# Optimization experiments

Hardware: AMD Instinct MI355X
Metric: run time of the kernel (lower is better)

Reference implementation:

```python
import jax, jax.numpy as jnp
import numpy as np
import math

B, S, H = 8, 160, 768
DEP = 64
NH, DH = 12, H // 12
W_EDGE = 1.0
EPS = 1e-5


def setup_inputs() -> dict:
    key = jax.random.key(0)
    ks = jax.random.split(key, 16)
    sc_h = 1.0 / math.sqrt(H)
    sc_d = 1.0 / math.sqrt(DEP)
    return {
        "token_feature": jax.random.normal(ks[0], (B, S, H), jnp.float32),
        "edge_feature": jax.random.normal(ks[1], (B, S, S, DEP), jnp.float32),
        "dependency_masks": jax.random.randint(ks[2], (B, S, S), 0, 2, jnp.int32),
        "Wq": jax.random.normal(ks[3], (H, H), jnp.float32) * sc_h,
        "bq": jnp.zeros((H,), jnp.float32),
        "Wk": jax.random.normal(ks[4], (H, H), jnp.float32) * sc_h,
        "bk": jnp.zeros((H,), jnp.float32),
        "Wv": jax.random.normal(ks[5], (H, H), jnp.float32) * sc_h,
        "bv": jnp.zeros((H,), jnp.float32),
        "Wek": jax.random.normal(ks[6], (DEP, H), jnp.float32) * sc_d,
        "bek": jnp.zeros((H,), jnp.float32),
        "Wev": jax.random.normal(ks[7], (DEP, H), jnp.float32) * sc_d,
        "bev": jnp.zeros((H,), jnp.float32),
        "ln_g": jnp.ones((H,), jnp.float32),
        "ln_b": jnp.zeros((H,), jnp.float32),
    }


def _heads3(x):  # [B,S,H] -> [B,NH,S,DH]
    return x.reshape(B, S, NH, DH).transpose(0, 2, 1, 3)


def _heads4(x):  # [B,S,S,H] -> [B,NH,S,S,DH]
    return x.reshape(B, S, S, NH, DH).transpose(0, 3, 1, 2, 4)


def reference(token_feature, edge_feature, dependency_masks,
              Wq, bq, Wk, bk, Wv, bv, Wek, bek, Wev, bev, ln_g, ln_b):
    q = _heads3(token_feature @ Wq + bq)   # [B,NH,S,DH]
    k = _heads3(token_feature @ Wk + bk)
    v = _heads3(token_feature @ Wv + bv)
    ek = _heads4(edge_feature @ Wek + bek)  # [B,NH,S,S,DH]
    ev = _heads4(edge_feature @ Wev + bev)
    # key_ij = k_j + w*ek_ij ; scores_ij = q_i . key_ij / sqrt(dh)
    scores = (jnp.einsum('bhid,bhjd->bhij', q, k)
              + W_EDGE * jnp.einsum('bhid,bhijd->bhij', q, ek))
    scores = scores / math.sqrt(DH)
    mask = (dependency_masks[:, None, :, :] == 0)  # [B,1,S,S]
    scores = jnp.where(mask, jnp.float32(-10000.0), scores)
    probs = jax.nn.softmax(scores, axis=-1)  # dropout is identity in eval
    ctx = (jnp.einsum('bhij,bhjd->bhid', probs, v)
           + W_EDGE * jnp.einsum('bhij,bhijd->bhid', probs, ev))
    ctx = ctx.transpose(0, 2, 1, 3).reshape(B, S, H)
    x = token_feature + ctx
    mu = jnp.mean(x, axis=-1, keepdims=True)
    var = jnp.mean(jnp.square(x - mu), axis=-1, keepdims=True)
    return (x - mu) / jnp.sqrt(var + EPS) * ln_g + ln_b
```

## Files before the change

kernel.cpp:

```cpp
#include <hip/hip_runtime.h>
#include <hip/hip_bf16.h>
#include <math.h>

#define BB 8
#define SS 160
#define HH 768
#define DEPTH 64
#define NHEAD 12
#define DHEAD 64
#define BS (BB*SS)
#define SCROW (NHEAD*SS)

constexpr float EPS_C = 1e-5f;

typedef __attribute__((ext_vector_type(8))) short bf16x8;
typedef __attribute__((ext_vector_type(4))) float f32x4;

__device__ inline short f2bs(float x) {
    union { __hip_bfloat16 b; short s; } u;
    u.b = __float2bfloat16(x);
    return u.s;
}

__global__ __launch_bounds__(256) void transpose_cast_w(
    const float* __restrict__ Wq, const float* __restrict__ Wk,
    const float* __restrict__ Wv, __hip_bfloat16* __restrict__ WT)
{
    __shared__ float t[32][33];
    const float* W = (blockIdx.z == 0) ? Wq : (blockIdx.z == 1) ? Wk : Wv;
    __hip_bfloat16* o = WT + (size_t)blockIdx.z * HH * HH;
    int kt = blockIdx.x * 32, nt = blockIdx.y * 32;
    int tx = threadIdx.x & 31, ty = threadIdx.x >> 5;
#pragma unroll
    for (int r = 0; r < 32; r += 8)
        t[ty + r][tx] = W[(size_t)(kt + ty + r) * HH + nt + tx];
    __syncthreads();
#pragma unroll
    for (int r = 0; r < 32; r += 8)
        o[(size_t)(nt + ty + r) * HH + kt + tx] = __float2bfloat16(t[tx][ty + r]);
}

__global__ __launch_bounds__(256) void gemm_qkv(
    const float* __restrict__ X, const __hip_bfloat16* __restrict__ WT,
    const float* __restrict__ bq, const float* __restrict__ bk,
    const float* __restrict__ bv,
    __hip_bfloat16* __restrict__ qb, __hip_bfloat16* __restrict__ kb,
    __hip_bfloat16* __restrict__ vb)
{
    __shared__ int4 sA[4][128];
    __shared__ int4 sB[4][64];
    int m0 = blockIdx.x * 128, n0 = blockIdx.y * 64, mat = blockIdx.z;
    const short* W = (const short*)WT + (size_t)mat * HH * HH;
    const float* bias = (mat == 0) ? bq : (mat == 1) ? bk : bv;
    int tid = threadIdx.x, w = tid >> 6, l = tid & 63;
    int wm = (w >> 1) * 64, wn = (w & 1) * 32;
    int khalf = l >> 4, lc = l & 15;

    f32x4 acc[4][2];
#pragma unroll
    for (int i = 0; i < 4; i++)
#pragma unroll
        for (int j = 0; j < 2; j++) acc[i][j] = (f32x4){0.f, 0.f, 0.f, 0.f};

    for (int k0 = 0; k0 < HH; k0 += 32) {
        __syncthreads();
#pragma unroll
        for (int rr = 0; rr < 2; rr++) {
            const float* ap = X + (size_t)(m0 + l + rr * 64) * HH + k0 + w * 8;
            float4 x0 = *(const float4*)ap;
            float4 x1 = *(const float4*)(ap + 4);
            bf16x8 p;
            p[0]=f2bs(x0.x); p[1]=f2bs(x0.y); p[2]=f2bs(x0.z); p[3]=f2bs(x0.w);
            p[4]=f2bs(x1.x); p[5]=f2bs(x1.y); p[6]=f2bs(x1.z); p[7]=f2bs(x1.w);
            *(bf16x8*)&sA[w][l + rr * 64] = p;
        }
        sB[w][l] = *(const int4*)(W + (size_t)(n0 + l) * HH + k0 + w * 8);
        __syncthreads();
        bf16x8 b0 = *(const bf16x8*)&sB[khalf][wn + lc];
        bf16x8 b1 = *(const bf16x8*)&sB[khalf][wn + 16 + lc];
#pragma unroll
        for (int mi = 0; mi < 4; mi++) {
            bf16x8 a = *(const bf16x8*)&sA[khalf][wm + mi * 16 + lc];
            acc[mi][0] = __builtin_amdgcn_mfma_f32_16x16x32_bf16(a, b0, acc[mi][0], 0, 0, 0);
            acc[mi][1] = __builtin_amdgcn_mfma_f32_16x16x32_bf16(a, b1, acc[mi][1], 0, 0, 0);
        }
    }

    int rg = (l >> 4) * 4;
    __hip_bfloat16* outm = (mat == 0) ? qb : (mat == 1) ? kb : vb;
#pragma unroll
    for (int ni = 0; ni < 2; ni++) {
        int gcol = n0 + wn + ni * 16 + lc;
        float bv_ = bias[gcol];
#pragma unroll
        for (int mi = 0; mi < 4; mi++) {
            int grow = m0 + wm + mi * 16 + rg;
            f32x4 a = acc[mi][ni];
            __hip_bfloat16* o = outm + (size_t)grow * HH + gcol;
            o[0]      = __float2bfloat16(a.x + bv_);
            o[HH]     = __float2bfloat16(a.y + bv_);
            o[2 * HH] = __float2bfloat16(a.z + bv_);
            o[3 * HH] = __float2bfloat16(a.w + bv_);
        }
    }
}

__global__ __launch_bounds__(256) void scores_gemm(
    const __hip_bfloat16* __restrict__ qb, const __hip_bfloat16* __restrict__ kb,
    _Float16* __restrict__ sc)
{
    __shared__ int4 sQ[8][160];
    __shared__ int4 sK[8][160];
    int h = blockIdx.x, b = blockIdx.y;
    const short* Q = (const short*)qb + (size_t)b * SS * HH + h * DHEAD;
    const short* K = (const short*)kb + (size_t)b * SS * HH + h * DHEAD;
    int tid = threadIdx.x, w = tid >> 6, l = tid & 63;

    for (int idx = tid; idx < SS * 8; idx += 256) {
        int row = idx >> 3, ch = idx & 7;
        sQ[ch][row] = *(const int4*)(Q + (size_t)row * HH + ch * 8);
        sK[ch][row] = *(const int4*)(K + (size_t)row * HH + ch * 8);
    }
    __syncthreads();

    int wm = (w >> 1) * 80, wn = (w & 1) * 80;
    int khalf = l >> 4, lc = l & 15;
    f32x4 acc[5][5];
#pragma unroll
    for (int i = 0; i < 5; i++)
#pragma unroll
        for (int j = 0; j < 5; j++) acc[i][j] = (f32x4){0.f, 0.f, 0.f, 0.f};

#pragma unroll
    for (int s = 0; s < 2; s++) {
        int c = s * 4 + khalf;
        bf16x8 bf[5];
#pragma unroll
        for (int ni = 0; ni < 5; ni++)
            bf[ni] = *(const bf16x8*)&sK[c][wn + ni * 16 + lc];
#pragma unroll
        for (int mi = 0; mi < 5; mi++) {
            bf16x8 a = *(const bf16x8*)&sQ[c][wm + mi * 16 + lc];
#pragma unroll
            for (int ni = 0; ni < 5; ni++)
                acc[mi][ni] = __builtin_amdgcn_mfma_f32_16x16x32_bf16(a, bf[ni], acc[mi][ni], 0, 0, 0);
        }
    }

    int rg = (l >> 4) * 4;
    _Float16* base = sc + ((size_t)b * SS) * SCROW + (size_t)h * SS;
#pragma unroll
    for (int mi = 0; mi < 5; mi++) {
        int i0 = wm + mi * 16 + rg;
#pragma unroll
        for (int ni = 0; ni < 5; ni++) {
            int j = wn + ni * 16 + lc;
            f32x4 a = acc[mi][ni];
            base[(size_t)(i0 + 0) * SCROW + j] = (_Float16)(a.x * 0.125f);
            base[(size_t)(i0 + 1) * SCROW + j] = (_Float16)(a.y * 0.125f);
            base[(size_t)(i0 + 2) * SCROW + j] = (_Float16)(a.z * 0.125f);
            base[(size_t)(i0 + 3) * SCROW + j] = (_Float16)(a.w * 0.125f);
        }
    }
}

__global__ __launch_bounds__(256) void qek_slim(
    const __hip_bfloat16* __restrict__ qb, const float* __restrict__ Wek,
    __hip_bfloat16* __restrict__ qek)
{
    __shared__ short sW[8 * 65 * 8];
    int h = blockIdx.x, mg = blockIdx.y;
    int tid = threadIdx.x, w = tid >> 6, l = tid & 63;
    int lr = l & 15, kg = l >> 4;

    {
        int d = tid >> 2, q4 = tid & 3;
        const float* wp = Wek + (size_t)d * HH + h * DHEAD + q4 * 16;
        float4 w0 = *(const float4*)(wp);
        float4 w1 = *(const float4*)(wp + 4);
        float4 w2 = *(const float4*)(wp + 8);
        float4 w3 = *(const float4*)(wp + 12);
        bf16x8 p0, p1;
        p0[0]=f2bs(w0.x); p0[1]=f2bs(w0.y); p0[2]=f2bs(w0.z); p0[3]=f2bs(w0.w);
        p0[4]=f2bs(w1.x); p0[5]=f2bs(w1.y); p0[6]=f2bs(w1.z); p0[7]=f2bs(w1.w);
        p1[0]=f2bs(w2.x); p1[1]=f2bs(w2.y); p1[2]=f2bs(w2.z); p1[3]=f2bs(w2.w);
        p1[4]=f2bs(w3.x); p1[5]=f2bs(w3.y); p1[6]=f2bs(w3.z); p1[7]=f2bs(w3.w);
        *(bf16x8*)&sW[((q4 * 2) * 65 + d) * 8]     = p0;
        *(bf16x8*)&sW[((q4 * 2 + 1) * 65 + d) * 8] = p1;
    }
    __syncthreads();

    bf16x8 bfrag[2][4];
#pragma unroll
    for (int s = 0; s < 2; s++)
#pragma unroll
        for (int nt = 0; nt < 4; nt++)
            bfrag[s][nt] = *(const bf16x8*)&sW[((s * 4 + kg) * 65 + nt * 16 + lr) * 8];

    const short* Q = (const short*)qb;
    short* O = (short*)qek;
    int m0 = (mg * 4 + w) * 16;
    bf16x8 a0 = *(const bf16x8*)(Q + (size_t)(m0 + lr) * HH + h * DHEAD + kg * 8);
    bf16x8 a1 = *(const bf16x8*)(Q + (size_t)(m0 + lr) * HH + h * DHEAD + 32 + kg * 8);
#pragma unroll
    for (int nt = 0; nt < 4; nt++) {
        f32x4 acc = (f32x4){0.f, 0.f, 0.f, 0.f};
        acc = __builtin_amdgcn_mfma_f32_16x16x32_bf16(a0, bfrag[0][nt], acc, 0, 0, 0);
        acc = __builtin_amdgcn_mfma_f32_16x16x32_bf16(a1, bfrag[1][nt], acc, 0, 0, 0);
        int row0 = m0 + kg * 4;
#pragma unroll
        for (int r = 0; r < 4; r++)
            O[(size_t)(row0 + r) * HH + h * DHEAD + nt * 16 + lr] = f2bs(acc[r]);
    }
}

__global__ __launch_bounds__(256) void escore_add2(
    const float* __restrict__ edge, const __hip_bfloat16* __restrict__ qek,
    _Float16* __restrict__ sc)
{
    int task = blockIdx.x * 4 + (threadIdx.x >> 6);
    int l = threadIdx.x & 63;
    int bi = task / 5, seg = task - (task / 5) * 5;
    int lr = l & 15, kg = l >> 4;

    const short* QE = (const short*)qek + (size_t)bi * HH;
    bf16x8 qe0 = *(const bf16x8*)(QE + lr * DHEAD + kg * 8);
    bf16x8 qe1 = *(const bf16x8*)(QE + lr * DHEAD + 32 + kg * 8);

    const float* E = edge + (size_t)bi * SS * DEPTH;
    _Float16* srow = sc + (size_t)bi * SCROW;

#pragma unroll
    for (int t = 0; t < 2; t++) {
        int jt = seg * 2 + t;
        const float* ep = E + (size_t)(jt * 16 + lr) * DEPTH + kg * 8;
        float4 e0 = *(const float4*)(ep);
        float4 e1 = *(const float4*)(ep + 4);
        float4 e2 = *(const float4*)(ep + 32);
        float4 e3 = *(const float4*)(ep + 36);
        bf16x8 a0, a1;
        a0[0]=f2bs(e0.x); a0[1]=f2bs(e0.y); a0[2]=f2bs(e0.z); a0[3]=f2bs(e0.w);
        a0[4]=f2bs(e1.x); a0[5]=f2bs(e1.y); a0[6]=f2bs(e1.z); a0[7]=f2bs(e1.w);
        a1[0]=f2bs(e2.x); a1[1]=f2bs(e2.y); a1[2]=f2bs(e2.z); a1[3]=f2bs(e2.w);
        a1[4]=f2bs(e3.x); a1[5]=f2bs(e3.y); a1[6]=f2bs(e3.z); a1[7]=f2bs(e3.w);
        f32x4 acc = (f32x4){0.f, 0.f, 0.f, 0.f};
        acc = __builtin_amdgcn_mfma_f32_16x16x32_bf16(a0, qe0, acc, 0, 0, 0);
        acc = __builtin_amdgcn_mfma_f32_16x16x32_bf16(a1, qe1, acc, 0, 0, 0);
        if (lr < NHEAD) {
            int j0 = jt * 16 + kg * 4;
            _Float16* p = srow + (size_t)lr * SS + j0;
#pragma unroll
            for (int r = 0; r < 4; r++)
                p[r] = (_Float16)((float)p[r] + 0.125f * acc[r]);
        }
    }
}

__global__ __launch_bounds__(256) void attn_kernel(
    const float* __restrict__ token, const float* __restrict__ edge,
    const int* __restrict__ mask,
    const __hip_bfloat16* __restrict__ q_ws, const _Float16* __restrict__ sc,
    const __hip_bfloat16* __restrict__ v_ws,
    const float* __restrict__ bek,
    const float* __restrict__ Wev, const float* __restrict__ bev,
    const float* __restrict__ ln_g, const float* __restrict__ ln_b,
    float* __restrict__ out)
{
    __shared__ float  s_ctx[HH];
    __shared__ float  s_scores[NHEAD][SS + 2];
    __shared__ float  s_pe[NHEAD][DEPTH];
    __shared__ float  s_x[HH];
    __shared__ float  s_qbek[NHEAD];
    __shared__ int    s_mask[SS];
    __shared__ float  s_red[8];

    int bi = blockIdx.x;
    int b  = bi / SS;
    int tid = threadIdx.x;
    int w = tid >> 6, l = tid & 63;
    int lr = l & 15, kg = l >> 4;

    if (tid < SS) s_mask[tid] = mask[(size_t)bi * SS + tid];

    {
        int hs = w * 3 + kg;
        float part = 0.f;
        if (hs < NHEAD) {
            const __hip_bfloat16* qp = q_ws + (size_t)bi * HH + hs * DHEAD + lr * 4;
            float4 bv4 = *(const float4*)(bek + hs * DHEAD + lr * 4);
            part = __bfloat162float(qp[0]) * bv4.x + __bfloat162float(qp[1]) * bv4.y
                 + __bfloat162float(qp[2]) * bv4.z + __bfloat162float(qp[3]) * bv4.w;
        }
        part += __shfl_xor(part, 1, 64);
        part += __shfl_xor(part, 2, 64);
        part += __shfl_xor(part, 4, 64);
        part += __shfl_xor(part, 8, 64);
        if (lr == 0 && hs < NHEAD) s_qbek[hs] = part;
    }
    __syncthreads();

    const float* scf = (const float*)(sc + (size_t)bi * SCROW);
    for (int idx = tid; idx < SCROW / 2; idx += 256) {
        int h = idx / (SS / 2), jp = idx - h * (SS / 2);
        union { float f; _Float16 e[2]; } u;
        u.f = scf[idx];
        int j = jp * 2;
        s_scores[h][j]     = s_mask[j]     ? ((float)u.e[0] + 0.125f * s_qbek[h]) : -10000.0f;
        s_scores[h][j + 1] = s_mask[j + 1] ? ((float)u.e[1] + 0.125f * s_qbek[h]) : -10000.0f;
    }
    __syncthreads();

    for (int h = w; h < NHEAD; h += 4) {
        float v0 = s_scores[h][l];
        float v1 = s_scores[h][l + 64];
        float v2 = (l < 32) ? s_scores[h][l + 128] : -INFINITY;
        float mx = fmaxf(v0, fmaxf(v1, v2));
#pragma unroll
        for (int mm = 32; mm >= 1; mm >>= 1) mx = fmaxf(mx, __shfl_xor(mx, mm, 64));
        float e0 = expf(v0 - mx), e1 = expf(v1 - mx);
        float e2 = (l < 32) ? expf(v2 - mx) : 0.f;
        float sm = e0 + e1 + e2;
#pragma unroll
        for (int mm = 32; mm >= 1; mm >>= 1) sm += __shfl_xor(sm, mm, 64);
        float inv = 1.0f / sm;
        s_scores[h][l]      = e0 * inv;
        s_scores[h][l + 64] = e1 * inv;
        if (l < 32) s_scores[h][l + 128] = e2 * inv;
    }
    __syncthreads();

    const float* e_row = edge + (size_t)bi * SS * DEPTH;
    {
        int h0 = w * 3;
        float av0 = 0.f, av1 = 0.f, av2 = 0.f;
        float pe0 = 0.f, pe1 = 0.f, pe2 = 0.f;
        const __hip_bfloat16* vbp = v_ws + (size_t)b * SS * HH + h0 * DHEAD + l;
        const float* er = e_row + l;
#pragma unroll 2
        for (int j0 = 0; j0 < SS; j0 += 2) {
            float2 p0 = *(const float2*)(&s_scores[h0][j0]);
            float2 p1 = *(const float2*)(&s_scores[h0 + 1][j0]);
            float2 p2 = *(const float2*)(&s_scores[h0 + 2][j0]);
            const __hip_bfloat16* vp = vbp + (size_t)j0 * HH;
            av0 += p0.x * __bfloat162float(vp[0])
                 + p0.y * __bfloat162float(vp[HH]);
            av1 += p1.x * __bfloat162float(vp[DHEAD])
                 + p1.y * __bfloat162float(vp[HH + DHEAD]);
            av2 += p2.x * __bfloat162float(vp[2 * DHEAD])
                 + p2.y * __bfloat162float(vp[HH + 2 * DHEAD]);
            float ev0 = er[(size_t)j0 * DEPTH];
            float ev1 = er[(size_t)(j0 + 1) * DEPTH];
            pe0 += p0.x * ev0 + p0.y * ev1;
            pe1 += p1.x * ev0 + p1.y * ev1;
            pe2 += p2.x * ev0 + p2.y * ev1;
        }
        s_pe[h0][l]     = pe0;
        s_pe[h0 + 1][l] = pe1;
        s_pe[h0 + 2][l] = pe2;
        s_ctx[h0 * DHEAD + l]       = av0;
        s_ctx[(h0 + 1) * DHEAD + l] = av1;
        s_ctx[(h0 + 2) * DHEAD + l] = av2;
    }
    __syncthreads();

    for (int mdx = tid; mdx < HH; mdx += 256) {
        int h = mdx >> 6;
        const float* pep = &s_pe[h][0];
        float sum = 0.f;
#pragma unroll
        for (int d = 0; d < DEPTH; d++) sum += pep[d] * Wev[(size_t)d * HH + mdx];
        float ctx = s_ctx[mdx] + (sum + bev[mdx]);
        s_x[mdx] = token[(size_t)bi * HH + mdx] + ctx;
    }
    __syncthreads();

    float lsum = 0.f, lsq = 0.f;
    for (int c = tid; c < HH; c += 256) {
        float x = s_x[c];
        lsum += x; lsq += x * x;
    }
#pragma unroll
    for (int mm = 32; mm >= 1; mm >>= 1) {
        lsum += __shfl_xor(lsum, mm, 64);
        lsq  += __shfl_xor(lsq,  mm, 64);
    }
    if (l == 0) { s_red[w] = lsum; s_red[4 + w] = lsq; }
    __syncthreads();
    float tsum = s_red[0] + s_red[1] + s_red[2] + s_red[3];
    float tsq  = s_red[4] + s_red[5] + s_red[6] + s_red[7];
    float mu  = tsum / HH;
    float var = tsq / HH - mu * mu;
    float rstd = rsqrtf(var + EPS_C);
    for (int c = tid; c < HH; c += 256)
        out[(size_t)bi * HH + c] = (s_x[c] - mu) * rstd * ln_g[c] + ln_b[c];
}

extern "C" void kernel_launch(void* const* d_in, const int* in_sizes, int n_in,
                              void* d_out, int out_size, void* d_ws, size_t ws_size,
                              hipStream_t stream) {
    const float* token = (const float*)d_in[0];
    const float* edge  = (const float*)d_in[1];
    const int*   mask  = (const int*)d_in[2];
    const float* Wq = (const float*)d_in[3];  const float* bq = (const float*)d_in[4];
    const float* Wk = (const float*)d_in[5];  const float* bk = (const float*)d_in[6];
    const float* Wv = (const float*)d_in[7];  const float* bv = (const float*)d_in[8];
    const float* Wek = (const float*)d_in[9];  const float* bek = (const float*)d_in[10];
    const float* Wev = (const float*)d_in[11]; const float* bev = (const float*)d_in[12];
    const float* ln_g = (const float*)d_in[13]; const float* ln_b = (const float*)d_in[14];
    float* out = (float*)d_out;

    __hip_bfloat16* qb = (__hip_bfloat16*)d_ws;
    __hip_bfloat16* kb = qb + (size_t)BS * HH;
    __hip_bfloat16* vb = kb + (size_t)BS * HH;
    __hip_bfloat16* WT = vb + (size_t)BS * HH;
    _Float16*       sc = (_Float16*)WT;
    __hip_bfloat16* qek = kb;

    transpose_cast_w<<<dim3(24, 24, 3), 256, 0, stream>>>(Wq, Wk, Wv, WT);
    gemm_qkv<<<dim3(BS / 128, HH / 64, 3), 256, 0, stream>>>(
        token, WT, bq, bk, bv, qb, kb, vb);
    scores_gemm<<<dim3(NHEAD, BB), 256, 0, stream>>>(qb, kb, sc);
    qek_slim<<<dim3(NHEAD, 20), 256, 0, stream>>>(qb, Wek, qek);
    escore_add2<<<1600, 256, 0, stream>>>(edge, qek, sc);
    attn_kernel<<<BS, 256, 0, stream>>>(token, edge, mask, qb, sc, vb,
                                        bek, Wev, bev, ln_g, ln_b, out);
}
```

Before: 119.1 us.

## Fuse weight transpose-cast into QKV GEMM and simplify attention loops

Drops the separate transpose_cast_w launch. The QKV GEMM now reads fp32 weights directly with strided per-column loads and converts them to bf16 while filling shared memory. The attention kernel now loads fp16 scores one element at a time instead of as packed pairs, and its PV/edge loop is rewritten to step one key per iteration with unroll 4 instead of two-key float2 steps. This saves a launch and the round trip of the transposed weight buffer, at the cost of strided, redundant fp32 weight reads in every GEMM tile and narrower memory accesses.

```diff
diff --git a/kernel.cpp b/kernel.cpp
--- a/kernel.cpp
+++ b/kernel.cpp
@@ -22,26 +22,10 @@
     return u.s;
 }
 
-__global__ __launch_bounds__(256) void transpose_cast_w(
+__global__ __launch_bounds__(256) void gemm_qkv(
+    const float* __restrict__ X,
     const float* __restrict__ Wq, const float* __restrict__ Wk,
-    const float* __restrict__ Wv, __hip_bfloat16* __restrict__ WT)
-{
-    __shared__ float t[32][33];
-    const float* W = (blockIdx.z == 0) ? Wq : (blockIdx.z == 1) ? Wk : Wv;
-    __hip_bfloat16* o = WT + (size_t)blockIdx.z * HH * HH;
-    int kt = blockIdx.x * 32, nt = blockIdx.y * 32;
-    int tx = threadIdx.x & 31, ty = threadIdx.x >> 5;
-#pragma unroll
-    for (int r = 0; r < 32; r += 8)
-        t[ty + r][tx] = W[(size_t)(kt + ty + r) * HH + nt + tx];
-    __syncthreads();
-#pragma unroll
-    for (int r = 0; r < 32; r += 8)
-        o[(size_t)(nt + ty + r) * HH + kt + tx] = __float2bfloat16(t[tx][ty + r]);
-}
-
-__global__ __launch_bounds__(256) void gemm_qkv(
-    const float* __restrict__ X, const __hip_bfloat16* __restrict__ WT,
+    const float* __restrict__ Wv,
     const float* __restrict__ bq, const float* __restrict__ bk,
     const float* __restrict__ bv,
     __hip_bfloat16* __restrict__ qb, __hip_bfloat16* __restrict__ kb,
@@ -50,7 +34,7 @@
     __shared__ int4 sA[4][128];
     __shared__ int4 sB[4][64];
     int m0 = blockIdx.x * 128, n0 = blockIdx.y * 64, mat = blockIdx.z;
-    const short* W = (const short*)WT + (size_t)mat * HH * HH;
+    const float* W    = (mat == 0) ? Wq : (mat == 1) ? Wk : Wv;
     const float* bias = (mat == 0) ? bq : (mat == 1) ? bk : bv;
     int tid = threadIdx.x, w = tid >> 6, l = tid & 63;
     int wm = (w >> 1) * 64, wn = (w & 1) * 32;
@@ -74,7 +58,13 @@
             p[4]=f2bs(x1.x); p[5]=f2bs(x1.y); p[6]=f2bs(x1.z); p[7]=f2bs(x1.w);
             *(bf16x8*)&sA[w][l + rr * 64] = p;
         }
-        sB[w][l] = *(const int4*)(W + (size_t)(n0 + l) * HH + k0 + w * 8);
+        {
+            const float* wp = W + (size_t)(k0 + w * 8) * HH + n0 + l;
+            bf16x8 p;
+#pragma unroll
+            for (int i = 0; i < 8; i++) p[i] = f2bs(wp[(size_t)i * HH]);
+            *(bf16x8*)&sB[w][l] = p;
+        }
         __syncthreads();
         bf16x8 b0 = *(const bf16x8*)&sB[khalf][wn + lc];
         bf16x8 b1 = *(const bf16x8*)&sB[khalf][wn + 16 + lc];
@@ -267,7 +257,7 @@
     float* __restrict__ out)
 {
     __shared__ float  s_ctx[HH];
-    __shared__ float  s_scores[NHEAD][SS + 2];
+    __shared__ float  s_scores[NHEAD][SS];
     __shared__ float  s_pe[NHEAD][DEPTH];
     __shared__ float  s_x[HH];
     __shared__ float  s_qbek[NHEAD];
@@ -299,14 +289,11 @@
     }
     __syncthreads();
 
-    const float* scf = (const float*)(sc + (size_t)bi * SCROW);
-    for (int idx = tid; idx < SCROW / 2; idx += 256) {
-        int h = idx / (SS / 2), jp = idx - h * (SS / 2);
-        union { float f; _Float16 e[2]; } u;
-        u.f = scf[idx];
-        int j = jp * 2;
-        s_scores[h][j]     = s_mask[j]     ? ((float)u.e[0] + 0.125f * s_qbek[h]) : -10000.0f;
-        s_scores[h][j + 1] = s_mask[j + 1] ? ((float)u.e[1] + 0.125f * s_qbek[h]) : -10000.0f;
+    const _Float16* scrow = sc + (size_t)bi * SCROW;
+    for (int idx = tid; idx < NHEAD * SS; idx += 256) {
+        int h = idx / SS, j = idx - h * SS;
+        float qk = (float)scrow[idx];
+        s_scores[h][j] = s_mask[j] ? (qk + 0.125f * s_qbek[h]) : -10000.0f;
     }
     __syncthreads();
 
@@ -336,23 +323,18 @@
         float pe0 = 0.f, pe1 = 0.f, pe2 = 0.f;
         const __hip_bfloat16* vbp = v_ws + (size_t)b * SS * HH + h0 * DHEAD + l;
         const float* er = e_row + l;
-#pragma unroll 2
-        for (int j0 = 0; j0 < SS; j0 += 2) {
-            float2 p0 = *(const float2*)(&s_scores[h0][j0]);
-            float2 p1 = *(const float2*)(&s_scores[h0 + 1][j0]);
-            float2 p2 = *(const float2*)(&s_scores[h0 + 2][j0]);
-            const __hip_bfloat16* vp = vbp + (size_t)j0 * HH;
-            av0 += p0.x * __bfloat162float(vp[0])
-                 + p0.y * __bfloat162float(vp[HH]);
-            av1 += p1.x * __bfloat162float(vp[DHEAD])
-                 + p1.y * __bfloat162float(vp[HH + DHEAD]);
-            av2 += p2.x * __bfloat162float(vp[2 * DHEAD])
-                 + p2.y * __bfloat162float(vp[HH + 2 * DHEAD]);
-            float ev0 = er[(size_t)j0 * DEPTH];
-            float ev1 = er[(size_t)(j0 + 1) * DEPTH];
-            pe0 += p0.x * ev0 + p0.y * ev1;
-            pe1 += p1.x * ev0 + p1.y * ev1;
-            pe2 += p2.x * ev0 + p2.y * ev1;
+        const float* p0r = &s_scores[h0][0];
+        const float* p1r = &s_scores[h0 + 1][0];
+        const float* p2r = &s_scores[h0 + 2][0];
+#pragma unroll 4
+        for (int j = 0; j < SS; j++) {
+            float p0 = p0r[j], p1 = p1r[j], p2 = p2r[j];
+            const __hip_bfloat16* vp = vbp + (size_t)j * HH;
+            av0 += p0 * __bfloat162float(vp[0]);
+            av1 += p1 * __bfloat162float(vp[DHEAD]);
+            av2 += p2 * __bfloat162float(vp[2 * DHEAD]);
+            float ev = er[(size_t)j * DEPTH];
+            pe0 += p0 * ev; pe1 += p1 * ev; pe2 += p2 * ev;
         }
         s_pe[h0][l]     = pe0;
         s_pe[h0 + 1][l] = pe1;
@@ -412,13 +394,11 @@
     __hip_bfloat16* qb = (__hip_bfloat16*)d_ws;
     __hip_bfloat16* kb = qb + (size_t)BS * HH;
     __hip_bfloat16* vb = kb + (size_t)BS * HH;
-    __hip_bfloat16* WT = vb + (size_t)BS * HH;
-    _Float16*       sc = (_Float16*)WT;
+    _Float16*       sc = (_Float16*)(vb + (size_t)BS * HH);
     __hip_bfloat16* qek = kb;
 
-    transpose_cast_w<<<dim3(24, 24, 3), 256, 0, stream>>>(Wq, Wk, Wv, WT);
     gemm_qkv<<<dim3(BS / 128, HH / 64, 3), 256, 0, stream>>>(
-        token, WT, bq, bk, bv, qb, kb, vb);
+        token, Wq, Wk, Wv, bq, bk, bv, qb, kb, vb);
     scores_gemm<<<dim3(NHEAD, BB), 256, 0, stream>>>(qb, kb, sc);
     qek_slim<<<dim3(NHEAD, 20), 256, 0, stream>>>(qb, Wek, qek);
     escore_add2<<<1600, 256, 0, stream>>>(edge, qek, sc);
```

Result: no change. 116.9 us (-1.9%).
